# Optimization experiments

Hardware: AMD Instinct MI355X
Metric: run time of the kernel (lower is better)

Reference implementation:

```python
import jax, jax.numpy as jnp
import numpy as np

B, N, M, Wlen = 4, 20000, 64, 8


def setup_inputs() -> dict:
    key = jax.random.key(0)
    k1, k2, k3, k4 = jax.random.split(key, 4)
    a0 = jax.random.uniform(k1, (B, N), dtype=jnp.float32)
    W = 0.01 * jax.random.normal(k2, (M, M), dtype=jnp.float32)
    X1 = jax.random.randint(k3, (M, N, Wlen, 2), 0, N, dtype=jnp.int64)
    X2 = jax.random.randint(k4, (M, N, Wlen, 2), 0, N, dtype=jnp.int64)
    return {"a0": a0, "W": W, "X1": X1, "X2": X2, "T": 2}


def f_clause_stack(a, X):
    # a: [B,n], X: [m,n,w,2] -> [B,m,n]
    y1 = a[:, X[..., 0]]  # [B,m,n,w] gather
    y2 = a[:, X[..., 1]]
    return jnp.max(y1 * y2, axis=3)


def predicate_forward(a, W, X1, X2, temperature=1.0):
    F1 = f_clause_stack(a, X1)  # [B,m1,n]
    F2 = f_clause_stack(a, X2)  # [B,m2,n]
    pi = jax.nn.softmax((W / temperature).reshape(-1)).reshape(W.shape)  # [m1,m2]
    pi1 = pi.sum(axis=1)  # [m1]
    pi2 = pi.sum(axis=0)  # [m2]
    Eu = jnp.einsum('j,bjn->bn', pi1, F1)
    Ev = jnp.einsum('k,bkn->bn', pi2, F2)
    Mt = jnp.einsum('jk,bkn->bjn', pi, F2)
    Euv = jnp.sum(F1 * Mt, axis=1)
    return Eu + Ev - Euv  # [B,n]


def reference(a0, W, X1, X2, T):
    a = a0
    for _ in range(T):  # T is a small static int
        derived = predicate_forward(a, W, X1, X2)
        # single intensional predicate -> stack/max over predicates is identity
        a = 1.0 - (1.0 - a) * (1.0 - derived)
    return a
```

## Files before the change

### kernel.cpp

```cpp
#include <hip/hip_runtime.h>

#define NN 20000

typedef _Float16 f16x2 __attribute__((ext_vector_type(2)));
typedef unsigned short u16x2 __attribute__((ext_vector_type(2)));

union U32H2 { unsigned int u; f16x2 h; };
union U32S2 { unsigned int u; u16x2 s; };

__device__ __forceinline__ f16x2 bc_h2(unsigned int u) { U32H2 x; x.u = u; return x.h; }
__device__ __forceinline__ unsigned int dup_h(float v) {
    _Float16 h = (_Float16)v;
    unsigned short b = __builtin_bit_cast(unsigned short, h);
    return ((unsigned int)b << 16) | b;
}
__device__ __forceinline__ unsigned int pkrtz_u32(float a, float b) {
    return __builtin_bit_cast(unsigned int, __builtin_amdgcn_cvt_pkrtz(a, b));
}

template <int CTRL>
__device__ __forceinline__ unsigned int pkmax_dpp(unsigned int v) {
    unsigned int d = (unsigned int)__builtin_amdgcn_update_dpp(
        0, (int)v, CTRL, 0xF, 0xF, true);
    U32S2 a, b; a.u = v; b.u = d;
    a.s = __builtin_elementwise_max(a.s, b.s);
    return a.u;
}
__device__ __forceinline__ unsigned int octmax_u16x2(unsigned int v) {
    v = pkmax_dpp<0xB1>(v);
    v = pkmax_dpp<0x4E>(v);
    v = pkmax_dpp<0x141>(v);
    return v;
}

__global__ __launch_bounds__(1024) void prep_kernel(const float* __restrict__ W,
                                                    unsigned int* __restrict__ pi_pk,
                                                    unsigned int* __restrict__ pi_t_pk,
                                                    unsigned int* __restrict__ pi1_pk,
                                                    unsigned int* __restrict__ pi2_pk) {
    __shared__ float red[1024];
    __shared__ float piL[4096];
    int t = threadIdx.x;
    float4 wv = ((const float4*)W)[t];
    float m = fmaxf(fmaxf(wv.x, wv.y), fmaxf(wv.z, wv.w));
    red[t] = m; __syncthreads();
    for (int s = 512; s > 0; s >>= 1) {
        if (t < s) red[t] = fmaxf(red[t], red[t + s]);
        __syncthreads();
    }
    m = red[0];
    __syncthreads();
    float e0 = expf(wv.x - m), e1 = expf(wv.y - m);
    float e2 = expf(wv.z - m), e3 = expf(wv.w - m);
    red[t] = e0 + e1 + e2 + e3;
    __syncthreads();
    for (int s = 512; s > 0; s >>= 1) {
        if (t < s) red[t] += red[t + s];
        __syncthreads();
    }
    float inv = 1.0f / red[0];
    float p[4] = { e0 * inv, e1 * inv, e2 * inv, e3 * inv };
#pragma unroll
    for (int i = 0; i < 4; i++) {
        int f = t * 4 + i;
        piL[f] = p[i];
        unsigned int d = dup_h(p[i]);
        pi_pk[f] = d;
        pi_t_pk[(f & 63) * 64 + (f >> 6)] = d;
    }
    __syncthreads();
    if (t < 64) {
        float s = 0.f;
        for (int k = 0; k < 64; k++) s += piL[t * 64 + k];
        pi1_pk[t] = dup_h(s);
    } else if (t < 128) {
        int k = t - 64;
        float s = 0.f;
        for (int j = 0; j < 64; j++) s += piL[j * 64 + k];
        pi2_pk[k] = dup_h(s);
    }
}

__global__ __launch_bounds__(1024) void pack_kernel(const float* __restrict__ a0,
                                                    unsigned int* __restrict__ T0) {
    int i = blockIdx.x * 1024 + threadIdx.x;
    if (i < NN) {
        unsigned int b0 = __float2uint_rn(__saturatef(a0[i]) * 255.0f);
        unsigned int b1 = __float2uint_rn(__saturatef(a0[NN + i]) * 255.0f);
        unsigned int b2 = __float2uint_rn(__saturatef(a0[2 * NN + i]) * 255.0f);
        unsigned int b3 = __float2uint_rn(__saturatef(a0[3 * NN + i]) * 255.0f);
        T0[i] = b0 | (b1 << 8) | (b2 << 16) | (b3 << 24);
    }
}

template <int ITER>
__global__ __launch_bounds__(1024, 4) void fused_iter(
    const unsigned int* __restrict__ Tsrc,
    const int* __restrict__ X1, const int* __restrict__ X2,
    const unsigned int* __restrict__ pi_t_pk,
    const unsigned int* __restrict__ pi1_pk,
    const unsigned int* __restrict__ pi2_pk,
    const float* __restrict__ a0,
    unsigned int* __restrict__ Tdst, float* __restrict__ outP) {
    __shared__ unsigned int tab[NN];
    __shared__ unsigned int Ft[128][40][2];
    __shared__ float redp[8][64][4];
    __shared__ float a_sm[64][4];

    const int t = threadIdx.x;
    for (int i = t; i < NN; i += 1024) tab[i] = Tsrc[i];

    const int bid = (int)blockIdx.x;
    const int bstart = bid < 32 ? bid * 79 : 32 * 79 + (bid - 32) * 78;
    const int bcnt = bid < 32 ? 79 : 78;
    const int c0 = (bcnt + 1) >> 1;

    const int wid = t >> 6, lane = t & 63, ni = lane >> 3, w = lane & 7;
    const int q = t >> 7, bp = (t >> 6) & 1, n_l = t & 63;
    const int widu = __builtin_amdgcn_readfirstlane(wid);
    const int qu = __builtin_amdgcn_readfirstlane(q);

    __syncthreads();

    for (int ch = 0; ch < 2; ++ch) {
        const int nb = bstart + (ch ? c0 : 0);
        const int cn = ch ? (bcnt - c0) : c0;

        {
            const float sc = 1.0f / 65025.0f;
            int loff[5];
#pragma unroll
            for (int oc = 0; oc < 5; ++oc) {
                int n = nb + oc * 8 + ni;
                int nc = n < NN ? n : NN - 1;
                loff[oc] = nc * 64 + w * 8;
            }
            int2 q5[5];
            {
                const int row = widu, k = row & 63;
                const char* Xb = (const char*)((row >> 6) ? X2 : X1)
                               + (unsigned)(k * NN) * 64u;
#pragma unroll
                for (int oc = 0; oc < 5; ++oc)
                    q5[oc] = *(const int2*)(Xb + loff[oc]);
            }
#pragma unroll
            for (int rr = 0; rr < 8; ++rr) {
                int2 qn[5];
                if (rr < 7) {
                    const int row = widu + 16 * (rr + 1), k = row & 63;
                    const char* Xb = (const char*)((row >> 6) ? X2 : X1)
                                   + (unsigned)(k * NN) * 64u;
#pragma unroll
                    for (int oc = 0; oc < 5; ++oc)
                        qn[oc] = *(const int2*)(Xb + loff[oc]);
                }
                const int row = widu + 16 * rr;
                unsigned int ga[5], gb[5];
#pragma unroll
                for (int oc = 0; oc < 5; ++oc) {
                    ga[oc] = tab[q5[oc].x];
                    gb[oc] = tab[q5[oc].y];
                }
#pragma unroll
                for (int oc = 0; oc < 5; ++oc) {
                    unsigned int ea = ga[oc] & 0x00FF00FFu;
                    unsigned int oa = (ga[oc] >> 8) & 0x00FF00FFu;
                    unsigned int eb = gb[oc] & 0x00FF00FFu;
                    unsigned int ob = (gb[oc] >> 8) & 0x00FF00FFu;
                    U32S2 pe, po, xb;
                    pe.u = ea; xb.u = eb; pe.s = pe.s * xb.s;
                    po.u = oa; xb.u = ob; po.s = po.s * xb.s;
                    unsigned int peu = octmax_u16x2(pe.u);
                    unsigned int pou = octmax_u16x2(po.u);
                    int col = oc * 8 + ni;
                    if (w == 0 && col < cn) {
                        float f0 = (float)(peu & 0xFFFFu) * sc;
                        float f1 = (float)(pou & 0xFFFFu) * sc;
                        float f2 = (float)(peu >> 16) * sc;
                        float f3 = (float)(pou >> 16) * sc;
                        unsigned int ul = pkrtz_u32(f0, f1);
                        unsigned int uh = pkrtz_u32(f2, f3);
                        *(uint2*)&Ft[row][col][0] = make_uint2(ul, uh);
                    }
                }
#pragma unroll
                for (int oc = 0; oc < 5; ++oc) q5[oc] = qn[oc];
            }
        }
        __syncthreads();

        {
            float part0 = 0.f, part1 = 0.f;
            if (n_l < cn) {
                f16x2 zero = {(_Float16)0, (_Float16)0};
                f16x2 f1v[8];
                f16x2 eu = zero;
#pragma unroll
                for (int jj = 0; jj < 8; ++jj) {
                    f1v[jj] = bc_h2(Ft[qu * 8 + jj][n_l][bp]);
                    eu += bc_h2(pi1_pk[qu * 8 + jj]) * f1v[jj];
                }
                f16x2 euv = zero, ev = zero;
#pragma unroll 8
                for (int k = 0; k < 64; ++k) {
                    f16x2 f2 = bc_h2(Ft[64 + k][n_l][bp]);
                    const uint4* pt = (const uint4*)(pi_t_pk + k * 64 + qu * 8);
                    uint4 w0 = pt[0], w1 = pt[1];
                    f16x2 ts = bc_h2(w0.x) * f1v[0] + bc_h2(w0.y) * f1v[1] +
                               bc_h2(w0.z) * f1v[2] + bc_h2(w0.w) * f1v[3] +
                               bc_h2(w1.x) * f1v[4] + bc_h2(w1.y) * f1v[5] +
                               bc_h2(w1.z) * f1v[6] + bc_h2(w1.w) * f1v[7];
                    euv += f2 * ts;
                    if (qu == 0) ev += bc_h2(pi2_pk[k]) * f2;
                }
                part0 = (float)eu[0] - (float)euv[0];
                part1 = (float)eu[1] - (float)euv[1];
                if (qu == 0) {
                    part0 += (float)ev[0];
                    part1 += (float)ev[1];
                }
            }
            *(float2*)&redp[q][n_l][bp * 2] = make_float2(part0, part1);
        }
        __syncthreads();

        if (t < 256) {
            int n = t & 63, b = t >> 6;
            if (n < cn) {
                float d = 0.f;
#pragma unroll
                for (int q8 = 0; q8 < 8; ++q8) d += redp[q8][n][b];
                int gn = nb + n;
                float ap;
                if (ITER == 1) ap = a0[(size_t)b * NN + gn];
                else ap = (float)((tab[gn] >> (8 * b)) & 255u) * (1.0f / 255.0f);
                float an = 1.0f - (1.0f - ap) * (1.0f - d);
                if (ITER == 1) a_sm[n][b] = an;
                else outP[(size_t)b * NN + gn] = an;
            }
        }
        __syncthreads();
        if (ITER == 1 && t < 64 && t < cn) {
            unsigned int b0 = __float2uint_rn(__saturatef(a_sm[t][0]) * 255.0f);
            unsigned int b1 = __float2uint_rn(__saturatef(a_sm[t][1]) * 255.0f);
            unsigned int b2 = __float2uint_rn(__saturatef(a_sm[t][2]) * 255.0f);
            unsigned int b3 = __float2uint_rn(__saturatef(a_sm[t][3]) * 255.0f);
            Tdst[nb + t] = b0 | (b1 << 8) | (b2 << 16) | (b3 << 24);
        }
        __syncthreads();
    }
}

extern "C" void kernel_launch(void* const* d_in, const int* in_sizes, int n_in,
                              void* d_out, int out_size, void* d_ws, size_t ws_size,
                              hipStream_t stream) {
    const float* a0 = (const float*)d_in[0];
    const float* W = (const float*)d_in[1];
    const int* X1 = (const int*)d_in[2];
    const int* X2 = (const int*)d_in[3];
    float* out = (float*)d_out;

    if (ws_size < (size_t)193280) return;
    unsigned int* pi_pk  = (unsigned int*)d_ws;
    unsigned int* pi_t   = (unsigned int*)((char*)d_ws + 16384);
    unsigned int* pi1_pk = (unsigned int*)((char*)d_ws + 32768);
    unsigned int* pi2_pk = (unsigned int*)((char*)d_ws + 33024);
    unsigned int* T0     = (unsigned int*)((char*)d_ws + 33280);
    unsigned int* T1     = (unsigned int*)((char*)d_ws + 113280);

    prep_kernel<<<1, 1024, 0, stream>>>(W, pi_pk, pi_t, pi1_pk, pi2_pk);
    pack_kernel<<<20, 1024, 0, stream>>>(a0, T0);
    fused_iter<1><<<256, 1024, 0, stream>>>(T0, X1, X2, pi_t, pi1_pk, pi2_pk,
                                            a0, T1, nullptr);
    fused_iter<2><<<256, 1024, 0, stream>>>(T1, X1, X2, pi_t, pi1_pk, pi2_pk,
                                            nullptr, nullptr, out);
}
```

Baseline: 250.0 us.

## Give each thread a whole clause row and merge setup kernels

The clause stage now maps each lane to one (row, node) pair and loads all eight index pairs with 16-byte int4 loads. It takes the max over the window inside the thread instead of reducing across eight lanes with DPP shuffles. Each thread issues 16 LDS table gathers per column, and byte extraction uses v_perm. The softmax prep and the a0 packing kernels are merged into one launch, and the unused pi_pk output is dropped. The cost is higher register pressure from the wider per-thread index buffers.

```diff
diff --git a/kernel.cpp b/kernel.cpp
--- a/kernel.cpp
+++ b/kernel.cpp
@@ -18,29 +18,26 @@
     return __builtin_bit_cast(unsigned int, __builtin_amdgcn_cvt_pkrtz(a, b));
 }
 
-template <int CTRL>
-__device__ __forceinline__ unsigned int pkmax_dpp(unsigned int v) {
-    unsigned int d = (unsigned int)__builtin_amdgcn_update_dpp(
-        0, (int)v, CTRL, 0xF, 0xF, true);
-    U32S2 a, b; a.u = v; b.u = d;
-    a.s = __builtin_elementwise_max(a.s, b.s);
-    return a.u;
-}
-__device__ __forceinline__ unsigned int octmax_u16x2(unsigned int v) {
-    v = pkmax_dpp<0xB1>(v);
-    v = pkmax_dpp<0x4E>(v);
-    v = pkmax_dpp<0x141>(v);
-    return v;
-}
-
-__global__ __launch_bounds__(1024) void prep_kernel(const float* __restrict__ W,
-                                                    unsigned int* __restrict__ pi_pk,
-                                                    unsigned int* __restrict__ pi_t_pk,
-                                                    unsigned int* __restrict__ pi1_pk,
-                                                    unsigned int* __restrict__ pi2_pk) {
+__global__ __launch_bounds__(1024) void setup_kernel(const float* __restrict__ W,
+                                                     const float* __restrict__ a0,
+                                                     unsigned int* __restrict__ pi_t_pk,
+                                                     unsigned int* __restrict__ pi1_pk,
+                                                     unsigned int* __restrict__ pi2_pk,
+                                                     unsigned int* __restrict__ T0) {
+    const int t = threadIdx.x;
+    if (blockIdx.x != 20) {
+        int i = blockIdx.x * 1024 + t;
+        if (i < NN) {
+            unsigned int b0 = __float2uint_rn(__saturatef(a0[i]) * 255.0f);
+            unsigned int b1 = __float2uint_rn(__saturatef(a0[NN + i]) * 255.0f);
+            unsigned int b2 = __float2uint_rn(__saturatef(a0[2 * NN + i]) * 255.0f);
+            unsigned int b3 = __float2uint_rn(__saturatef(a0[3 * NN + i]) * 255.0f);
+            T0[i] = b0 | (b1 << 8) | (b2 << 16) | (b3 << 24);
+        }
+        return;
+    }
     __shared__ float red[1024];
     __shared__ float piL[4096];
-    int t = threadIdx.x;
     float4 wv = ((const float4*)W)[t];
     float m = fmaxf(fmaxf(wv.x, wv.y), fmaxf(wv.z, wv.w));
     red[t] = m; __syncthreads();
@@ -64,9 +61,7 @@
     for (int i = 0; i < 4; i++) {
         int f = t * 4 + i;
         piL[f] = p[i];
-        unsigned int d = dup_h(p[i]);
-        pi_pk[f] = d;
-        pi_t_pk[(f & 63) * 64 + (f >> 6)] = d;
+        pi_t_pk[(f & 63) * 64 + (f >> 6)] = dup_h(p[i]);
     }
     __syncthreads();
     if (t < 64) {
@@ -78,18 +73,6 @@
         float s = 0.f;
         for (int j = 0; j < 64; j++) s += piL[j * 64 + k];
         pi2_pk[k] = dup_h(s);
-    }
-}
-
-__global__ __launch_bounds__(1024) void pack_kernel(const float* __restrict__ a0,
-                                                    unsigned int* __restrict__ T0) {
-    int i = blockIdx.x * 1024 + threadIdx.x;
-    if (i < NN) {
-        unsigned int b0 = __float2uint_rn(__saturatef(a0[i]) * 255.0f);
-        unsigned int b1 = __float2uint_rn(__saturatef(a0[NN + i]) * 255.0f);
-        unsigned int b2 = __float2uint_rn(__saturatef(a0[2 * NN + i]) * 255.0f);
-        unsigned int b3 = __float2uint_rn(__saturatef(a0[3 * NN + i]) * 255.0f);
-        T0[i] = b0 | (b1 << 8) | (b2 << 16) | (b3 << 24);
     }
 }
 
@@ -115,10 +98,16 @@
     const int bcnt = bid < 32 ? 79 : 78;
     const int c0 = (bcnt + 1) >> 1;
 
-    const int wid = t >> 6, lane = t & 63, ni = lane >> 3, w = lane & 7;
+    const int wid = t >> 6, lane = t & 63;
+    const int widu = __builtin_amdgcn_readfirstlane(wid);
+    const int r8 = lane >> 3, n8 = lane & 7;
+    const int row = widu * 8 + r8;
+    const int k = row & 63;
     const int q = t >> 7, bp = (t >> 6) & 1, n_l = t & 63;
-    const int widu = __builtin_amdgcn_readfirstlane(wid);
     const int qu = __builtin_amdgcn_readfirstlane(q);
+
+    const char* Xrow = (const char*)(widu >= 8 ? X2 : X1)
+                     + (size_t)((unsigned)(k * NN)) * 64u;
 
     __syncthreads();
 
@@ -131,61 +120,51 @@
             int loff[5];
 #pragma unroll
             for (int oc = 0; oc < 5; ++oc) {
-                int n = nb + oc * 8 + ni;
+                int n = nb + oc * 8 + n8;
                 int nc = n < NN ? n : NN - 1;
-                loff[oc] = nc * 64 + w * 8;
-            }
-            int2 q5[5];
-            {
-                const int row = widu, k = row & 63;
-                const char* Xb = (const char*)((row >> 6) ? X2 : X1)
-                               + (unsigned)(k * NN) * 64u;
-#pragma unroll
-                for (int oc = 0; oc < 5; ++oc)
-                    q5[oc] = *(const int2*)(Xb + loff[oc]);
-            }
-#pragma unroll
-            for (int rr = 0; rr < 8; ++rr) {
-                int2 qn[5];
-                if (rr < 7) {
-                    const int row = widu + 16 * (rr + 1), k = row & 63;
-                    const char* Xb = (const char*)((row >> 6) ? X2 : X1)
-                                   + (unsigned)(k * NN) * 64u;
-#pragma unroll
-                    for (int oc = 0; oc < 5; ++oc)
-                        qn[oc] = *(const int2*)(Xb + loff[oc]);
-                }
-                const int row = widu + 16 * rr;
-                unsigned int ga[5], gb[5];
-#pragma unroll
-                for (int oc = 0; oc < 5; ++oc) {
-                    ga[oc] = tab[q5[oc].x];
-                    gb[oc] = tab[q5[oc].y];
-                }
-#pragma unroll
-                for (int oc = 0; oc < 5; ++oc) {
-                    unsigned int ea = ga[oc] & 0x00FF00FFu;
-                    unsigned int oa = (ga[oc] >> 8) & 0x00FF00FFu;
-                    unsigned int eb = gb[oc] & 0x00FF00FFu;
-                    unsigned int ob = (gb[oc] >> 8) & 0x00FF00FFu;
+                loff[oc] = nc * 64;
+            }
+            int4 qa[4], qb[4];
+#pragma unroll
+            for (int i = 0; i < 4; ++i) qa[i] = *(const int4*)(Xrow + loff[0] + i * 16);
+
+#pragma unroll
+            for (int oc = 0; oc < 5; ++oc) {
+                if (oc < 4) {
+#pragma unroll
+                    for (int i = 0; i < 4; ++i)
+                        qb[i] = *(const int4*)(Xrow + loff[oc + 1] + i * 16);
+                }
+                unsigned int g[16];
+                const int* qi = (const int*)qa;
+#pragma unroll
+                for (int p = 0; p < 16; ++p) g[p] = tab[qi[p]];
+
+                U32S2 me, mo; me.u = 0u; mo.u = 0u;
+#pragma unroll
+                for (int p = 0; p < 8; ++p) {
+                    unsigned int ax = g[2 * p], bx = g[2 * p + 1];
+                    unsigned int ea = ax & 0x00FF00FFu;
+                    unsigned int oa = __builtin_amdgcn_perm(0u, ax, 0x0C030C01u);
+                    unsigned int eb = bx & 0x00FF00FFu;
+                    unsigned int ob = __builtin_amdgcn_perm(0u, bx, 0x0C030C01u);
                     U32S2 pe, po, xb;
                     pe.u = ea; xb.u = eb; pe.s = pe.s * xb.s;
                     po.u = oa; xb.u = ob; po.s = po.s * xb.s;
-                    unsigned int peu = octmax_u16x2(pe.u);
-                    unsigned int pou = octmax_u16x2(po.u);
-                    int col = oc * 8 + ni;
-                    if (w == 0 && col < cn) {
-                        float f0 = (float)(peu & 0xFFFFu) * sc;
-                        float f1 = (float)(pou & 0xFFFFu) * sc;
-                        float f2 = (float)(peu >> 16) * sc;
-                        float f3 = (float)(pou >> 16) * sc;
-                        unsigned int ul = pkrtz_u32(f0, f1);
-                        unsigned int uh = pkrtz_u32(f2, f3);
-                        *(uint2*)&Ft[row][col][0] = make_uint2(ul, uh);
-                    }
-                }
-#pragma unroll
-                for (int oc = 0; oc < 5; ++oc) q5[oc] = qn[oc];
+                    me.s = __builtin_elementwise_max(me.s, pe.s);
+                    mo.s = __builtin_elementwise_max(mo.s, po.s);
+                }
+                int col = oc * 8 + n8;
+                if (col < cn) {
+                    float f0 = (float)(me.u & 0xFFFFu) * sc;
+                    float f1 = (float)(mo.u & 0xFFFFu) * sc;
+                    float f2 = (float)(me.u >> 16) * sc;
+                    float f3 = (float)(mo.u >> 16) * sc;
+                    *(uint2*)&Ft[row][col][0] =
+                        make_uint2(pkrtz_u32(f0, f1), pkrtz_u32(f2, f3));
+                }
+#pragma unroll
+                for (int i = 0; i < 4; ++i) qa[i] = qb[i];
             }
         }
         __syncthreads();
@@ -203,16 +182,16 @@
                 }
                 f16x2 euv = zero, ev = zero;
 #pragma unroll 8
-                for (int k = 0; k < 64; ++k) {
-                    f16x2 f2 = bc_h2(Ft[64 + k][n_l][bp]);
-                    const uint4* pt = (const uint4*)(pi_t_pk + k * 64 + qu * 8);
+                for (int k2 = 0; k2 < 64; ++k2) {
+                    f16x2 f2 = bc_h2(Ft[64 + k2][n_l][bp]);
+                    const uint4* pt = (const uint4*)(pi_t_pk + k2 * 64 + qu * 8);
                     uint4 w0 = pt[0], w1 = pt[1];
                     f16x2 ts = bc_h2(w0.x) * f1v[0] + bc_h2(w0.y) * f1v[1] +
                                bc_h2(w0.z) * f1v[2] + bc_h2(w0.w) * f1v[3] +
                                bc_h2(w1.x) * f1v[4] + bc_h2(w1.y) * f1v[5] +
                                bc_h2(w1.z) * f1v[6] + bc_h2(w1.w) * f1v[7];
                     euv += f2 * ts;
-                    if (qu == 0) ev += bc_h2(pi2_pk[k]) * f2;
+                    if (qu == 0) ev += bc_h2(pi2_pk[k2]) * f2;
                 }
                 part0 = (float)eu[0] - (float)euv[0];
                 part1 = (float)eu[1] - (float)euv[1];
@@ -262,15 +241,13 @@
     float* out = (float*)d_out;
 
     if (ws_size < (size_t)193280) return;
-    unsigned int* pi_pk  = (unsigned int*)d_ws;
     unsigned int* pi_t   = (unsigned int*)((char*)d_ws + 16384);
     unsigned int* pi1_pk = (unsigned int*)((char*)d_ws + 32768);
     unsigned int* pi2_pk = (unsigned int*)((char*)d_ws + 33024);
     unsigned int* T0     = (unsigned int*)((char*)d_ws + 33280);
     unsigned int* T1     = (unsigned int*)((char*)d_ws + 113280);
 
-    prep_kernel<<<1, 1024, 0, stream>>>(W, pi_pk, pi_t, pi1_pk, pi2_pk);
-    pack_kernel<<<20, 1024, 0, stream>>>(a0, T0);
+    setup_kernel<<<21, 1024, 0, stream>>>(W, a0, pi_t, pi1_pk, pi2_pk, T0);
     fused_iter<1><<<256, 1024, 0, stream>>>(T0, X1, X2, pi_t, pi1_pk, pi2_pk,
                                             a0, T1, nullptr);
     fused_iter<2><<<256, 1024, 0, stream>>>(T1, X1, X2, pi_t, pi1_pk, pi2_pk,
```

Measured after the change: 243.4 us. 1.03x faster.
